# Kernel optimization log

Hardware: AMD Instinct MI355X
Metric: run time of the kernel (lower is better)

## Reference

```python
import jax, jax.numpy as jnp
import numpy as np

D = 768   # embedding_len
NL = 4    # nleft attributes
NR = 4    # nright attributes
LL = 256  # total left tokens
LR = 256  # total right tokens
DE = (NL + NR) * D  # entity-matching highway width


def setup_inputs() -> dict:
    key = jax.random.key(0)
    ks = jax.random.split(key, 12)
    f = lambda k, s: (jax.random.normal(k, s, jnp.float32) * 0.02)
    return {
        "left_emb": jax.random.normal(ks[0], (LL, D), jnp.float32),
        "right_emb": jax.random.normal(ks[1], (LR, D), jnp.float32),
        "Wn_tok": f(ks[2], (D, D)), "bn_tok": jnp.zeros((D,), jnp.float32),
        "Wg_tok": f(ks[3], (D, D)), "bg_tok": jnp.full((D,), -2.0, jnp.float32),
        "W_lin_tok": f(ks[4], (D, 1)), "b_lin_tok": jnp.zeros((1,), jnp.float32),
        "attr_emb_left": f(ks[5], (NL, D)),
        "attr_emb_right": f(ks[6], (NR, D)),
        "Wn_ent": f(ks[7], (DE, DE)), "bn_ent": jnp.zeros((DE,), jnp.float32),
        "Wg_ent": f(ks[8], (DE, DE)), "bg_ent": jnp.full((DE,), -2.0, jnp.float32),
        "W_lin_ent": f(ks[9], (DE, 2)), "b_lin_ent": jnp.zeros((2,), jnp.float32),
        "empty_attr_res": f(ks[10], (D,)),
        # per-attribute token counts; left includes an empty attribute
        "left_attrs_len": jnp.array([100, 80, 76, 0], dtype=jnp.int32),
        "right_attrs_len": jnp.array([64, 64, 64, 64], dtype=jnp.int32),
    }


def _highway(x, Wn, bn, Wg, bg):
    h = jax.nn.relu(x @ Wn + bn)
    g = jax.nn.sigmoid(x @ Wg + bg)
    return h * g + (1.0 - g) * x


def _token_matching(left, right, Wn, bn, Wg, bg, W_lin, b_lin):
    # compare_matrix: [L_left, L_right, D]
    cmp = jnp.abs(left[:, None, :] - right[None, :, :])
    hw = _highway(cmp, Wn, bn, Wg, bg)
    scores = hw @ W_lin + b_lin                     # [Ll, Lr, 1]
    # softmax over dim=1 (right tokens); only argmax is used downstream
    idx = jnp.argmax(scores[..., 0], axis=1)        # [Ll]
    return jnp.take_along_axis(cmp, idx[:, None, None], axis=1)[:, 0, :]  # [Ll, D]


def _attribute_matching(tokens, field_emb, cmp_res, lens, empty_attr):
    # ragged per-attribute softmax-weighted segment reduction
    n = field_emb.shape[0]
    L = tokens.shape[0]
    seg = jnp.repeat(jnp.arange(n), lens, total_repeat_length=L)   # [L]
    scores = jnp.einsum('ld,ld->l', tokens, field_emb[seg])        # [L]
    m = jax.ops.segment_max(scores, seg, num_segments=n)
    e = jnp.exp(scores - m[seg])
    z = jax.ops.segment_sum(e, seg, num_segments=n)
    w = e / z[seg]                                                  # softmax within segment
    reps = jax.ops.segment_sum(w[:, None] * cmp_res, seg, num_segments=n)  # [n, D]
    return jnp.where(lens[:, None] > 0, reps, empty_attr[None, :])


def reference(left_emb, right_emb, Wn_tok, bn_tok, Wg_tok, bg_tok,
              W_lin_tok, b_lin_tok, attr_emb_left, attr_emb_right,
              Wn_ent, bn_ent, Wg_ent, bg_ent, W_lin_ent, b_lin_ent,
              empty_attr_res, left_attrs_len, right_attrs_len):
    left_cmp = _token_matching(left_emb, right_emb, Wn_tok, bn_tok, Wg_tok, bg_tok,
                               W_lin_tok, b_lin_tok)
    right_cmp = _token_matching(right_emb, left_emb, Wn_tok, bn_tok, Wg_tok, bg_tok,
                                W_lin_tok, b_lin_tok)
    left_rep = _attribute_matching(left_emb, attr_emb_left, left_cmp,
                                   left_attrs_len, empty_attr_res)
    right_rep = _attribute_matching(right_emb, attr_emb_right, right_cmp,
                                    right_attrs_len, empty_attr_res)
    concat = jnp.concatenate([left_rep, right_rep], axis=0).reshape(1, -1)  # [1, DE]
    hw = _highway(concat, Wn_ent, bn_ent, Wg_ent, bg_ent)
    logits = hw @ W_lin_ent + b_lin_ent                                     # [1, 2]
    return jax.nn.softmax(logits, axis=1).flatten()                         # [2]
```

## Files before the change

### kernel.cpp

```cpp
#include <hip/hip_runtime.h>
#include <math.h>
#include <stdint.h>

#define DD 768
#define NT 256
#define DE 6144

typedef _Float16 half8 __attribute__((ext_vector_type(8)));
typedef _Float16 half4 __attribute__((ext_vector_type(4)));
typedef short short8 __attribute__((ext_vector_type(8)));
typedef float floatx4 __attribute__((ext_vector_type(4)));

__device__ __forceinline__ void async_ld16(const void* g, void* l) {
  __builtin_amdgcn_global_load_lds(
      (const __attribute__((address_space(1))) unsigned int*)g,
      (__attribute__((address_space(3))) unsigned int*)l, 16, 0, 0);
}

__device__ __forceinline__ unsigned ordf(float f) {
  unsigned u = __float_as_uint(f);
  return (u & 0x80000000u) ? ~u : (u | 0x80000000u);
}

__global__ __launch_bounds__(256) void prep(
    const float* __restrict__ Wn, const float* __restrict__ Wg,
    _Float16* __restrict__ WnT, _Float16* __restrict__ WgT,
    const float* __restrict__ L, const float* __restrict__ R,
    _Float16* __restrict__ Lh, _Float16* __restrict__ Rh)
{
  const int b = blockIdx.x;
  if (b < 1152) {
    const int z = b / 576;
    const int by = (b / 24) % 24;
    const int bx = b % 24;
    const float* W = z ? Wg : Wn;
    _Float16* WT = z ? WgT : WnT;
    __shared__ float tile[32][33];
    const int tx = threadIdx.x & 31, ty = threadIdx.x >> 5;
    const int d0 = bx * 32, k0 = by * 32;
    #pragma unroll
    for (int p = 0; p < 4; ++p)
      tile[ty + p*8][tx] = W[(size_t)(k0 + ty + p*8)*DD + d0 + tx];
    __syncthreads();
    #pragma unroll
    for (int p = 0; p < 4; ++p) {
      const int d = d0 + ty + p*8;
      const int k = k0 + tx;
      const int idx = d*DD + (k & ~63) + ((((k >> 3) & 7) ^ (d & 7)) << 3) + (k & 7);
      WT[idx] = (_Float16)tile[tx][ty + p*8];
    }
  } else {
    const int c = b - 1152;
    const int side = c / 192;
    const float* src = side ? R : L;
    _Float16* dst = side ? Rh : Lh;
    const int o = (c % 192)*1024 + threadIdx.x*4;
    float4 v = *(const float4*)&src[o];
    half4 h; h[0] = (_Float16)v.x; h[1] = (_Float16)v.y;
    h[2] = (_Float16)v.z; h[3] = (_Float16)v.w;
    *(half4*)&dst[o] = h;
  }
}

__global__ __launch_bounds__(512, 1) void score_mfma(
    const _Float16* __restrict__ Lh, const _Float16* __restrict__ Rh,
    const _Float16* __restrict__ WnT, const _Float16* __restrict__ WgT,
    const float* __restrict__ bn, const float* __restrict__ bg,
    const float* __restrict__ Wl, float* __restrict__ Sp)
{
  const int dbase = blockIdx.x * 128;
  const int i     = blockIdx.y;
  const int tid   = threadIdx.x;

  __shared__ _Float16 As [2][256*64];
  __shared__ _Float16 Bns[2][128*64];
  __shared__ _Float16 Bgs[2][128*64];

  floatx4 accn[4][4] = {};
  floatx4 accg[4][4] = {};

  const int kg = tid & 7;
  const int rl = tid >> 3;

  const int lane = tid & 63;
  const int wid  = tid >> 6;
  const int wj = (wid & 3) * 64;
  const int wd = (wid >> 2) * 64;
  const int m = lane & 15;
  const int q = lane >> 4;
  const int gq8 = ((q ^ (m & 7)) << 3);

  const int drow = lane >> 3;
  const int dseg = lane & 7;

  int arow[4], brow[4];
  #pragma unroll
  for (int t4 = 0; t4 < 4; ++t4) {
    arow[t4] = (wj + t4*16 + m) * 64;
    brow[t4] = (wd + t4*16 + m) * 64;
  }

  auto stageB = [&](int k0, int c) {
    #pragma unroll
    for (int tt = 0; tt < 2; ++tt) {
      const int brow0 = wid*16 + tt*8;
      async_ld16(&WnT[(size_t)(dbase + brow0 + drow)*DD + k0 + dseg*8],
                 &Bns[c][brow0*64]);
      async_ld16(&WgT[(size_t)(dbase + brow0 + drow)*DD + k0 + dseg*8],
                 &Bgs[c][brow0*64]);
    }
  };

  stageB(0, 0);
  {
    half8 lh0 = *(const half8*)&Lh[i*DD + kg*8];
    #pragma unroll
    for (int rep = 0; rep < 4; ++rep) {
      const int row = rl + rep*64;
      half8 rv0 = *(const half8*)&Rh[(size_t)row*DD + kg*8];
      half8 dv8 = lh0 - rv0;
      short8 sb; __builtin_memcpy(&sb, &dv8, 16);
      sb &= (short)0x7FFF;
      *(short8*)&As[0][row*64 + ((kg ^ (row & 7)) << 3)] = sb;
    }
  }
  __syncthreads();

  for (int t = 0; t < 12; ++t) {
    const int cur = t & 1;
    const bool st = (t < 11);
    const int k0n = (t + 1) * 64;

    half8 rv[4], lh;
    if (st) {
      stageB(k0n, cur ^ 1);
      __builtin_amdgcn_sched_barrier(0);
      lh = *(const half8*)&Lh[i*DD + k0n + kg*8];
      #pragma unroll
      for (int rep = 0; rep < 4; ++rep)
        rv[rep] = *(const half8*)&Rh[(size_t)(rl + rep*64)*DD + k0n + kg*8];
      __builtin_amdgcn_sched_barrier(0);
    }

    half8 af[4][2];
    #pragma unroll
    for (int tj = 0; tj < 4; ++tj)
      #pragma unroll
      for (int kk = 0; kk < 2; ++kk)
        af[tj][kk] = *(const half8*)&As[cur][arow[tj] + ((kk*32) ^ gq8)];
    __builtin_amdgcn_s_setprio(1);
    #pragma unroll
    for (int td = 0; td < 4; ++td) {
      half8 bn_[2], bg_[2];
      #pragma unroll
      for (int kk = 0; kk < 2; ++kk) {
        bn_[kk] = *(const half8*)&Bns[cur][brow[td] + ((kk*32) ^ gq8)];
        bg_[kk] = *(const half8*)&Bgs[cur][brow[td] + ((kk*32) ^ gq8)];
      }
      #pragma unroll
      for (int kk = 0; kk < 2; ++kk)
        #pragma unroll
        for (int tj = 0; tj < 4; ++tj) {
          accn[tj][td] = __builtin_amdgcn_mfma_f32_16x16x32_f16(
              af[tj][kk], bn_[kk], accn[tj][td], 0, 0, 0);
          accg[tj][td] = __builtin_amdgcn_mfma_f32_16x16x32_f16(
              af[tj][kk], bg_[kk], accg[tj][td], 0, 0, 0);
        }
    }
    __builtin_amdgcn_s_setprio(0);

    if (st) {
      #pragma unroll
      for (int rep = 0; rep < 4; ++rep) {
        const int row = rl + rep*64;
        half8 dv8 = lh - rv[rep];
        short8 sb; __builtin_memcpy(&sb, &dv8, 16);
        sb &= (short)0x7FFF;
        *(short8*)&As[cur ^ 1][row*64 + ((kg ^ (row & 7)) << 3)] = sb;
      }
    }
    __syncthreads();
  }

  float bnv[4], bgv[4], wlv[4], lv[4];
  int dv[4];
  #pragma unroll
  for (int td = 0; td < 4; ++td) {
    const int d = dbase + wd + td*16 + m;
    dv[td] = d; bnv[td] = bn[d]; bgv[td] = bg[d]; wlv[td] = Wl[d];
    lv[td] = (float)Lh[i*DD + d];
  }
  const int jb = wj;
  const int plane = blockIdx.x * 2 + (wid >> 2);
  float* Sout = Sp + (size_t)plane * NT * NT + (size_t)i * NT;
  #pragma unroll
  for (int tj = 0; tj < 4; ++tj) {
    #pragma unroll
    for (int r = 0; r < 4; ++r) {
      const int j = jb + tj*16 + q*4 + r;
      float sc = 0.f;
      #pragma unroll
      for (int td = 0; td < 4; ++td) {
        const float nv = accn[tj][td][r] + bnv[td];
        const float gp = accg[tj][td][r] + bgv[td];
        const float g  = 1.f / (1.f + __expf(-gp));
        const float c  = fabsf(lv[td] - (float)Rh[(size_t)j*DD + dv[td]]);
        sc += (fmaxf(nv, 0.f)*g + (1.f - g)*c) * wlv[td];
      }
      sc += __shfl_xor(sc, 1, 16);
      sc += __shfl_xor(sc, 2, 16);
      sc += __shfl_xor(sc, 4, 16);
      sc += __shfl_xor(sc, 8, 16);
      if (m == 0) Sout[j] = sc;
    }
  }
}

__global__ __launch_bounds__(256) void argmax_attr(
    const float* __restrict__ Sp,
    int* __restrict__ idxL, unsigned long long* __restrict__ colKey,
    const float* __restrict__ Lemb, const float* __restrict__ Remb,
    const float* __restrict__ AEl, const float* __restrict__ AEr,
    const int* __restrict__ lensL, const int* __restrict__ lensR,
    float* __restrict__ wS, int* __restrict__ segA)
{
  const int b = blockIdx.x;
  const int t = threadIdx.x;

  if (b < NT) {
    const size_t off = (size_t)b*NT + t;
    float v = 0.f;
    #pragma unroll
    for (int p = 0; p < 12; ++p) v += Sp[(size_t)p*NT*NT + off];
    const unsigned long long key =
        ((unsigned long long)ordf(v) << 32) | (unsigned)(NT - 1 - b);
    atomicMax(&colKey[t], key);
    int idx = t;
    #pragma unroll
    for (int mm = 1; mm < 64; mm <<= 1) {
      float ov = __shfl_xor(v, mm, 64);
      int   oi = __shfl_xor(idx, mm, 64);
      if (ov > v || (ov == v && oi < idx)) { v = ov; idx = oi; }
    }
    __shared__ float sv[4]; __shared__ int si[4];
    if ((t & 63) == 0) { sv[t>>6] = v; si[t>>6] = idx; }
    __syncthreads();
    if (t == 0) {
      #pragma unroll
      for (int w = 1; w < 4; ++w)
        if (sv[w] > v || (sv[w] == v && si[w] < idx)) { v = sv[w]; idx = si[w]; }
      idxL[b] = idx;
    }
    return;
  }

  const int side = b - NT;
  const float* tok = side ? Remb : Lemb;
  const float* AE  = side ? AEr  : AEl;
  const int* lens  = side ? lensR : lensL;
  const int c0 = lens[0], c1 = c0 + lens[1], c2 = c1 + lens[2];
  const int seg = (t < c0) ? 0 : (t < c1) ? 1 : (t < c2) ? 2 : 3;
  float s = 0.f;
  const float4* tr = (const float4*)&tok[(size_t)t*DD];
  const float4* ar = (const float4*)&AE[(size_t)seg*DD];
  for (int k = 0; k < DD/4; ++k) {
    float4 a = tr[k], bb = ar[k];
    s += a.x*bb.x + a.y*bb.y + a.z*bb.z + a.w*bb.w;
  }
  __shared__ float scS[NT]; __shared__ int segS[NT];
  __shared__ float mS[4], zS[4];
  scS[t] = s; segS[t] = seg;
  __syncthreads();
  if (t < 4) {
    float mx = -INFINITY;
    for (int u = 0; u < NT; ++u) if (segS[u] == t) mx = fmaxf(mx, scS[u]);
    mS[t] = mx;
    float z = 0.f;
    for (int u = 0; u < NT; ++u) if (segS[u] == t) z += __expf(scS[u] - mx);
    zS[t] = z;
  }
  __syncthreads();
  wS[side*NT + t] = __expf(s - mS[seg]) / zS[seg];
  segA[side*NT + t] = seg;
}

__global__ __launch_bounds__(256) void attr_reduce(
    const float* __restrict__ Lemb, const float* __restrict__ Remb,
    const int* __restrict__ lensL, const int* __restrict__ lensR,
    const int* __restrict__ idxL, const unsigned long long* __restrict__ colKey,
    const float* __restrict__ wS, const int* __restrict__ segA,
    const float* __restrict__ empty, float* __restrict__ x)
{
  const int side = blockIdx.x;
  const float* tok = side ? Remb : Lemb;
  const float* oth = side ? Lemb : Remb;
  const int* lens  = side ? lensR : lensL;
  const float* w   = wS + side*NT;
  const int* sg    = segA + side*NT;
  float* xo = x + side*4*DD;
  const int t = threadIdx.x;
  const int dl = t & 63, uq = t >> 6;
  const int d = blockIdx.y*64 + dl;
  float a0 = 0.f, a1 = 0.f, a2 = 0.f, a3 = 0.f;
  for (int u = uq*64; u < uq*64 + 64; ++u) {
    const int iu = side ? (NT - 1 - (int)(unsigned)(colKey[u] & 0xffffffffULL))
                        : idxL[u];
    const float c = fabsf(tok[(size_t)u*DD + d] - oth[(size_t)iu*DD + d]);
    const float wc = w[u] * c;
    const int s = sg[u];
    a0 += (s == 0) ? wc : 0.f;
    a1 += (s == 1) ? wc : 0.f;
    a2 += (s == 2) ? wc : 0.f;
    a3 += (s == 3) ? wc : 0.f;
  }
  __shared__ float red[4][4][64];
  red[uq][0][dl] = a0; red[uq][1][dl] = a1;
  red[uq][2][dl] = a2; red[uq][3][dl] = a3;
  __syncthreads();
  if (uq == 0) {
    #pragma unroll
    for (int s = 0; s < 4; ++s) {
      float v = red[0][s][dl] + red[1][s][dl] + red[2][s][dl] + red[3][s][dl];
      xo[s*DD + d] = (lens[s] > 0) ? v : empty[d];
    }
  }
}

__global__ __launch_bounds__(256) void ent_matvec4(
    const float* __restrict__ x,
    const float* __restrict__ Wn, const float* __restrict__ Wg,
    float* __restrict__ pn, float* __restrict__ pg)
{
  const float* W = blockIdx.z ? Wg : Wn;
  float* p = blockIdx.z ? pg : pn;
  __shared__ float xs[96];
  const int db = blockIdx.x;
  const int kb = blockIdx.y;
  const int tid = threadIdx.x;
  if (tid < 96) xs[tid] = x[kb*96 + tid];
  __syncthreads();
  const int col = db*1024 + tid*4;
  float4 a = {0.f,0.f,0.f,0.f};
  const size_t base = (size_t)kb*96*DE + col;
  #pragma unroll 8
  for (int kk = 0; kk < 96; ++kk) {
    const float xv = xs[kk];
    float4 w = *(const float4*)&W[base + (size_t)kk*DE];
    a.x = fmaf(xv, w.x, a.x); a.y = fmaf(xv, w.y, a.y);
    a.z = fmaf(xv, w.z, a.z); a.w = fmaf(xv, w.w, a.w);
  }
  *(float4*)&p[(size_t)kb*DE + col] = a;
}

__global__ __launch_bounds__(256) void ent_reduce(
    const float* __restrict__ pn, const float* __restrict__ pg,
    float* __restrict__ yn, float* __restrict__ yg)
{
  const int o = blockIdx.x*256 + threadIdx.x;
  float sn = 0.f, sg = 0.f;
  for (int kb = 0; kb < 64; ++kb) {
    sn += pn[(size_t)kb*DE + o];
    sg += pg[(size_t)kb*DE + o];
  }
  yn[o] = sn; yg[o] = sg;
}

__global__ __launch_bounds__(256) void final_kernel(
    const float* __restrict__ x, const float* __restrict__ yn,
    const float* __restrict__ yg, const float* __restrict__ bn,
    const float* __restrict__ bg, const float* __restrict__ Wl,
    const float* __restrict__ bl, float* __restrict__ out)
{
  const int tid = threadIdx.x;
  float a0 = 0.f, a1 = 0.f;
  for (int p = 0; p < DE/256; ++p) {
    int d = p*256 + tid;
    float n  = yn[d] + bn[d];
    float gp = yg[d] + bg[d];
    float h  = fmaxf(n, 0.f);
    float g  = 1.f / (1.f + __expf(-gp));
    float hw = h*g + (1.f - g)*x[d];
    a0 += hw * Wl[d*2 + 0];
    a1 += hw * Wl[d*2 + 1];
  }
  #pragma unroll
  for (int mm = 1; mm < 64; mm <<= 1) {
    a0 += __shfl_xor(a0, mm, 64);
    a1 += __shfl_xor(a1, mm, 64);
  }
  __shared__ float s0[4], s1[4];
  if ((tid & 63) == 0) { s0[tid>>6] = a0; s1[tid>>6] = a1; }
  __syncthreads();
  if (tid == 0) {
    for (int w = 1; w < 4; ++w) { a0 += s0[w]; a1 += s1[w]; }
    float l0 = a0 + bl[0], l1 = a1 + bl[1];
    float m = fmaxf(l0, l1);
    float e0 = __expf(l0 - m), e1 = __expf(l1 - m);
    out[0] = e0 / (e0 + e1);
    out[1] = e1 / (e0 + e1);
  }
}

extern "C" void kernel_launch(void* const* d_in, const int* in_sizes, int n_in,
                              void* d_out, int out_size, void* d_ws, size_t ws_size,
                              hipStream_t stream) {
  const float* Lemb   = (const float*)d_in[0];
  const float* Remb   = (const float*)d_in[1];
  const float* Wn_tok = (const float*)d_in[2];
  const float* bn_tok = (const float*)d_in[3];
  const float* Wg_tok = (const float*)d_in[4];
  const float* bg_tok = (const float*)d_in[5];
  const float* Wl_tok = (const float*)d_in[6];
  const float* AEl    = (const float*)d_in[8];
  const float* AEr    = (const float*)d_in[9];
  const float* Wn_ent = (const float*)d_in[10];
  const float* bn_ent = (const float*)d_in[11];
  const float* Wg_ent = (const float*)d_in[12];
  const float* bg_ent = (const float*)d_in[13];
  const float* Wl_ent = (const float*)d_in[14];
  const float* bl_ent = (const float*)d_in[15];
  const float* empty  = (const float*)d_in[16];
  const int*   lensL  = (const int*)d_in[17];
  const int*   lensR  = (const int*)d_in[18];

  char* ws = (char*)d_ws;
  float* Sp   = (float*)(ws + 0);
  float* pn   = (float*)(ws + 0);
  float* pg   = (float*)(ws + 1572864);
  unsigned long long* colKey = (unsigned long long*)(ws + 3145728);
  float* x    = (float*)(ws + 3147776);
  float* yn   = (float*)(ws + 3172352);
  float* yg   = (float*)(ws + 3196928);
  float* wSm  = (float*)(ws + 3221504);
  int*  segA  = (int*)  (ws + 3223552);
  _Float16* WnT = (_Float16*)(ws + 3225600);
  _Float16* WgT = (_Float16*)(ws + 4405248);
  _Float16* Lh  = (_Float16*)(ws + 5584896);
  _Float16* Rh  = (_Float16*)(ws + 5978112);
  int* idxL = (int*)(ws + 3225600);

  prep<<<1536, 256, 0, stream>>>(Wn_tok, Wg_tok, WnT, WgT, Lemb, Remb, Lh, Rh);
  hipMemsetAsync(colKey, 0, 2048, stream);
  score_mfma<<<dim3(6, 256), 512, 0, stream>>>(
      Lh, Rh, WnT, WgT, bn_tok, bg_tok, Wl_tok, Sp);
  argmax_attr<<<NT + 2, 256, 0, stream>>>(
      Sp, idxL, colKey, Lemb, Remb, AEl, AEr, lensL, lensR, wSm, segA);
  attr_reduce<<<dim3(2, 12), 256, 0, stream>>>(
      Lemb, Remb, lensL, lensR, idxL, colKey, wSm, segA, empty, x);
  ent_matvec4<<<dim3(6, 64, 2), 256, 0, stream>>>(x, Wn_ent, Wg_ent, pn, pg);
  ent_reduce<<<24, 256, 0, stream>>>(pn, pg, yn, yg);
  final_kernel<<<1, 256, 0, stream>>>(
      x, yn, yg, bn_ent, bg_ent, Wl_ent, bl_ent, (float*)d_out);
}
```

Measured before the change: 664.0 us.

## Fuse tail kernels into one cooperative kernel with grid syncs

Replaces the five tail launches (argmax/attr scores, attr_reduce, entity matvec, reduce, final) with a single cooperative kernel of 512 blocks that separates the stages with grid.sync. It also folds the colKey memset into the prep kernel. The aim is to remove launch gaps and a memset call. In exchange it adds grid-wide barrier overhead, and the work is spread over fewer blocks, e.g. the matvec now runs 768 work items on 512 blocks.

```diff
diff --git a/kernel.cpp b/kernel.cpp
--- a/kernel.cpp
+++ b/kernel.cpp
@@ -1,10 +1,13 @@
 #include <hip/hip_runtime.h>
+#include <hip/hip_cooperative_groups.h>
 #include <math.h>
 #include <stdint.h>
 
 #define DD 768
 #define NT 256
 #define DE 6144
+
+namespace cg = cooperative_groups;
 
 typedef _Float16 half8 __attribute__((ext_vector_type(8)));
 typedef _Float16 half4 __attribute__((ext_vector_type(4)));
@@ -26,7 +29,8 @@
     const float* __restrict__ Wn, const float* __restrict__ Wg,
     _Float16* __restrict__ WnT, _Float16* __restrict__ WgT,
     const float* __restrict__ L, const float* __restrict__ R,
-    _Float16* __restrict__ Lh, _Float16* __restrict__ Rh)
+    _Float16* __restrict__ Lh, _Float16* __restrict__ Rh,
+    unsigned long long* __restrict__ colKey)
 {
   const int b = blockIdx.x;
   if (b < 1152) {
@@ -50,6 +54,7 @@
       WT[idx] = (_Float16)tile[tx][ty + p*8];
     }
   } else {
+    if (b == 1152) colKey[threadIdx.x] = 0ULL;
     const int c = b - 1152;
     const int side = c / 192;
     const float* src = side ? R : L;
@@ -216,16 +221,31 @@
   }
 }
 
-__global__ __launch_bounds__(256) void argmax_attr(
+__global__ __launch_bounds__(256) void tail_coop(
     const float* __restrict__ Sp,
     int* __restrict__ idxL, unsigned long long* __restrict__ colKey,
     const float* __restrict__ Lemb, const float* __restrict__ Remb,
     const float* __restrict__ AEl, const float* __restrict__ AEr,
     const int* __restrict__ lensL, const int* __restrict__ lensR,
-    float* __restrict__ wS, int* __restrict__ segA)
+    float* __restrict__ wS, int* __restrict__ segA,
+    const float* __restrict__ empty, float* __restrict__ x,
+    const float* __restrict__ Wn_ent, const float* __restrict__ Wg_ent,
+    float* __restrict__ pn, float* __restrict__ pg,
+    float* __restrict__ yn, float* __restrict__ yg,
+    const float* __restrict__ bn_ent, const float* __restrict__ bg_ent,
+    const float* __restrict__ Wl_ent, const float* __restrict__ bl_ent,
+    float* __restrict__ out)
 {
+  cg::grid_group grid = cg::this_grid();
   const int b = blockIdx.x;
   const int t = threadIdx.x;
+
+  __shared__ float sv[4]; __shared__ int si[4];
+  __shared__ float scS[NT]; __shared__ int segS[NT];
+  __shared__ float mS[4], zS[4];
+  __shared__ float red[4][4][64];
+  __shared__ float xs[96];
+  __shared__ float s0[4], s1[4];
 
   if (b < NT) {
     const size_t off = (size_t)b*NT + t;
@@ -242,7 +262,6 @@
       int   oi = __shfl_xor(idx, mm, 64);
       if (ov > v || (ov == v && oi < idx)) { v = ov; idx = oi; }
     }
-    __shared__ float sv[4]; __shared__ int si[4];
     if ((t & 63) == 0) { sv[t>>6] = v; si[t>>6] = idx; }
     __syncthreads();
     if (t == 0) {
@@ -251,153 +270,142 @@
         if (sv[w] > v || (sv[w] == v && si[w] < idx)) { v = sv[w]; idx = si[w]; }
       idxL[b] = idx;
     }
-    return;
-  }
-
-  const int side = b - NT;
-  const float* tok = side ? Remb : Lemb;
-  const float* AE  = side ? AEr  : AEl;
-  const int* lens  = side ? lensR : lensL;
-  const int c0 = lens[0], c1 = c0 + lens[1], c2 = c1 + lens[2];
-  const int seg = (t < c0) ? 0 : (t < c1) ? 1 : (t < c2) ? 2 : 3;
-  float s = 0.f;
-  const float4* tr = (const float4*)&tok[(size_t)t*DD];
-  const float4* ar = (const float4*)&AE[(size_t)seg*DD];
-  for (int k = 0; k < DD/4; ++k) {
-    float4 a = tr[k], bb = ar[k];
-    s += a.x*bb.x + a.y*bb.y + a.z*bb.z + a.w*bb.w;
-  }
-  __shared__ float scS[NT]; __shared__ int segS[NT];
-  __shared__ float mS[4], zS[4];
-  scS[t] = s; segS[t] = seg;
-  __syncthreads();
-  if (t < 4) {
-    float mx = -INFINITY;
-    for (int u = 0; u < NT; ++u) if (segS[u] == t) mx = fmaxf(mx, scS[u]);
-    mS[t] = mx;
-    float z = 0.f;
-    for (int u = 0; u < NT; ++u) if (segS[u] == t) z += __expf(scS[u] - mx);
-    zS[t] = z;
-  }
-  __syncthreads();
-  wS[side*NT + t] = __expf(s - mS[seg]) / zS[seg];
-  segA[side*NT + t] = seg;
-}
-
-__global__ __launch_bounds__(256) void attr_reduce(
-    const float* __restrict__ Lemb, const float* __restrict__ Remb,
-    const int* __restrict__ lensL, const int* __restrict__ lensR,
-    const int* __restrict__ idxL, const unsigned long long* __restrict__ colKey,
-    const float* __restrict__ wS, const int* __restrict__ segA,
-    const float* __restrict__ empty, float* __restrict__ x)
-{
-  const int side = blockIdx.x;
-  const float* tok = side ? Remb : Lemb;
-  const float* oth = side ? Lemb : Remb;
-  const int* lens  = side ? lensR : lensL;
-  const float* w   = wS + side*NT;
-  const int* sg    = segA + side*NT;
-  float* xo = x + side*4*DD;
-  const int t = threadIdx.x;
-  const int dl = t & 63, uq = t >> 6;
-  const int d = blockIdx.y*64 + dl;
-  float a0 = 0.f, a1 = 0.f, a2 = 0.f, a3 = 0.f;
-  for (int u = uq*64; u < uq*64 + 64; ++u) {
-    const int iu = side ? (NT - 1 - (int)(unsigned)(colKey[u] & 0xffffffffULL))
-                        : idxL[u];
-    const float c = fabsf(tok[(size_t)u*DD + d] - oth[(size_t)iu*DD + d]);
-    const float wc = w[u] * c;
-    const int s = sg[u];
-    a0 += (s == 0) ? wc : 0.f;
-    a1 += (s == 1) ? wc : 0.f;
-    a2 += (s == 2) ? wc : 0.f;
-    a3 += (s == 3) ? wc : 0.f;
-  }
-  __shared__ float red[4][4][64];
-  red[uq][0][dl] = a0; red[uq][1][dl] = a1;
-  red[uq][2][dl] = a2; red[uq][3][dl] = a3;
-  __syncthreads();
-  if (uq == 0) {
-    #pragma unroll
-    for (int s = 0; s < 4; ++s) {
-      float v = red[0][s][dl] + red[1][s][dl] + red[2][s][dl] + red[3][s][dl];
-      xo[s*DD + d] = (lens[s] > 0) ? v : empty[d];
-    }
-  }
-}
-
-__global__ __launch_bounds__(256) void ent_matvec4(
-    const float* __restrict__ x,
-    const float* __restrict__ Wn, const float* __restrict__ Wg,
-    float* __restrict__ pn, float* __restrict__ pg)
-{
-  const float* W = blockIdx.z ? Wg : Wn;
-  float* p = blockIdx.z ? pg : pn;
-  __shared__ float xs[96];
-  const int db = blockIdx.x;
-  const int kb = blockIdx.y;
-  const int tid = threadIdx.x;
-  if (tid < 96) xs[tid] = x[kb*96 + tid];
-  __syncthreads();
-  const int col = db*1024 + tid*4;
-  float4 a = {0.f,0.f,0.f,0.f};
-  const size_t base = (size_t)kb*96*DE + col;
-  #pragma unroll 8
-  for (int kk = 0; kk < 96; ++kk) {
-    const float xv = xs[kk];
-    float4 w = *(const float4*)&W[base + (size_t)kk*DE];
-    a.x = fmaf(xv, w.x, a.x); a.y = fmaf(xv, w.y, a.y);
-    a.z = fmaf(xv, w.z, a.z); a.w = fmaf(xv, w.w, a.w);
-  }
-  *(float4*)&p[(size_t)kb*DE + col] = a;
-}
-
-__global__ __launch_bounds__(256) void ent_reduce(
-    const float* __restrict__ pn, const float* __restrict__ pg,
-    float* __restrict__ yn, float* __restrict__ yg)
-{
-  const int o = blockIdx.x*256 + threadIdx.x;
-  float sn = 0.f, sg = 0.f;
-  for (int kb = 0; kb < 64; ++kb) {
-    sn += pn[(size_t)kb*DE + o];
-    sg += pg[(size_t)kb*DE + o];
-  }
-  yn[o] = sn; yg[o] = sg;
-}
-
-__global__ __launch_bounds__(256) void final_kernel(
-    const float* __restrict__ x, const float* __restrict__ yn,
-    const float* __restrict__ yg, const float* __restrict__ bn,
-    const float* __restrict__ bg, const float* __restrict__ Wl,
-    const float* __restrict__ bl, float* __restrict__ out)
-{
-  const int tid = threadIdx.x;
-  float a0 = 0.f, a1 = 0.f;
-  for (int p = 0; p < DE/256; ++p) {
-    int d = p*256 + tid;
-    float n  = yn[d] + bn[d];
-    float gp = yg[d] + bg[d];
-    float h  = fmaxf(n, 0.f);
-    float g  = 1.f / (1.f + __expf(-gp));
-    float hw = h*g + (1.f - g)*x[d];
-    a0 += hw * Wl[d*2 + 0];
-    a1 += hw * Wl[d*2 + 1];
-  }
+  } else if (b < NT + 2) {
+    const int side = b - NT;
+    const float* tok = side ? Remb : Lemb;
+    const float* AE  = side ? AEr  : AEl;
+    const int* lens  = side ? lensR : lensL;
+    const int c0 = lens[0], c1 = c0 + lens[1], c2 = c1 + lens[2];
+    const int seg = (t < c0) ? 0 : (t < c1) ? 1 : (t < c2) ? 2 : 3;
+    float s = 0.f;
+    const float4* tr = (const float4*)&tok[(size_t)t*DD];
+    const float4* ar = (const float4*)&AE[(size_t)seg*DD];
+    for (int k = 0; k < DD/4; ++k) {
+      float4 a = tr[k], bb = ar[k];
+      s += a.x*bb.x + a.y*bb.y + a.z*bb.z + a.w*bb.w;
+    }
+    scS[t] = s; segS[t] = seg;
+    __syncthreads();
+    if (t < 4) {
+      float mx = -INFINITY;
+      for (int u = 0; u < NT; ++u) if (segS[u] == t) mx = fmaxf(mx, scS[u]);
+      mS[t] = mx;
+      float z = 0.f;
+      for (int u = 0; u < NT; ++u) if (segS[u] == t) z += __expf(scS[u] - mx);
+      zS[t] = z;
+    }
+    __syncthreads();
+    wS[side*NT + t] = __expf(s - mS[seg]) / zS[seg];
+    segA[side*NT + t] = seg;
+  }
+  __threadfence();
+  grid.sync();
+
+  if (b < 24) {
+    const int side = b & 1;
+    const int dblk = b >> 1;
+    const float* tok = side ? Remb : Lemb;
+    const float* oth = side ? Lemb : Remb;
+    const int* lens  = side ? lensR : lensL;
+    const float* w   = wS + side*NT;
+    const int* sg    = segA + side*NT;
+    float* xo = x + side*4*DD;
+    const int dl = t & 63, uq = t >> 6;
+    const int d = dblk*64 + dl;
+    float a0 = 0.f, a1 = 0.f, a2 = 0.f, a3 = 0.f;
+    for (int u = uq*64; u < uq*64 + 64; ++u) {
+      const int iu = side ? (NT - 1 - (int)(unsigned)(colKey[u] & 0xffffffffULL))
+                          : idxL[u];
+      const float c = fabsf(tok[(size_t)u*DD + d] - oth[(size_t)iu*DD + d]);
+      const float wc = w[u] * c;
+      const int s = sg[u];
+      a0 += (s == 0) ? wc : 0.f;
+      a1 += (s == 1) ? wc : 0.f;
+      a2 += (s == 2) ? wc : 0.f;
+      a3 += (s == 3) ? wc : 0.f;
+    }
+    red[uq][0][dl] = a0; red[uq][1][dl] = a1;
+    red[uq][2][dl] = a2; red[uq][3][dl] = a3;
+    __syncthreads();
+    if (uq == 0) {
+      #pragma unroll
+      for (int s = 0; s < 4; ++s) {
+        float v = red[0][s][dl] + red[1][s][dl] + red[2][s][dl] + red[3][s][dl];
+        xo[s*DD + d] = (lens[s] > 0) ? v : empty[d];
+      }
+    }
+  }
+  __threadfence();
+  grid.sync();
+
   #pragma unroll
-  for (int mm = 1; mm < 64; mm <<= 1) {
-    a0 += __shfl_xor(a0, mm, 64);
-    a1 += __shfl_xor(a1, mm, 64);
-  }
-  __shared__ float s0[4], s1[4];
-  if ((tid & 63) == 0) { s0[tid>>6] = a0; s1[tid>>6] = a1; }
-  __syncthreads();
-  if (tid == 0) {
-    for (int w = 1; w < 4; ++w) { a0 += s0[w]; a1 += s1[w]; }
-    float l0 = a0 + bl[0], l1 = a1 + bl[1];
-    float m = fmaxf(l0, l1);
-    float e0 = __expf(l0 - m), e1 = __expf(l1 - m);
-    out[0] = e0 / (e0 + e1);
-    out[1] = e1 / (e0 + e1);
+  for (int rep = 0; rep < 2; ++rep) {
+    const int u = b + rep*512;
+    if (u < 768) {
+      const int mat = u / 384;
+      const int rem = u % 384;
+      const int kb  = rem / 6;
+      const int db  = rem % 6;
+      const float* W = mat ? Wg_ent : Wn_ent;
+      float* p = mat ? pg : pn;
+      __syncthreads();
+      if (t < 96) xs[t] = x[kb*96 + t];
+      __syncthreads();
+      const int col = db*1024 + t*4;
+      float4 a = {0.f,0.f,0.f,0.f};
+      const size_t base = (size_t)kb*96*DE + col;
+      #pragma unroll 8
+      for (int kk = 0; kk < 96; ++kk) {
+        const float xv = xs[kk];
+        float4 w = *(const float4*)&W[base + (size_t)kk*DE];
+        a.x = fmaf(xv, w.x, a.x); a.y = fmaf(xv, w.y, a.y);
+        a.z = fmaf(xv, w.z, a.z); a.w = fmaf(xv, w.w, a.w);
+      }
+      *(float4*)&p[(size_t)kb*DE + col] = a;
+    }
+  }
+  __threadfence();
+  grid.sync();
+
+  if (b < 24) {
+    const int o = b*256 + t;
+    float sn = 0.f, sg = 0.f;
+    for (int kb = 0; kb < 64; ++kb) {
+      sn += pn[(size_t)kb*DE + o];
+      sg += pg[(size_t)kb*DE + o];
+    }
+    yn[o] = sn; yg[o] = sg;
+  }
+  __threadfence();
+  grid.sync();
+
+  if (b == 0) {
+    float a0 = 0.f, a1 = 0.f;
+    for (int p = 0; p < DE/256; ++p) {
+      int d = p*256 + t;
+      float n  = yn[d] + bn_ent[d];
+      float gp = yg[d] + bg_ent[d];
+      float h  = fmaxf(n, 0.f);
+      float g  = 1.f / (1.f + __expf(-gp));
+      float hw = h*g + (1.f - g)*x[d];
+      a0 += hw * Wl_ent[d*2 + 0];
+      a1 += hw * Wl_ent[d*2 + 1];
+    }
+    #pragma unroll
+    for (int mm = 1; mm < 64; mm <<= 1) {
+      a0 += __shfl_xor(a0, mm, 64);
+      a1 += __shfl_xor(a1, mm, 64);
+    }
+    if ((t & 63) == 0) { s0[t>>6] = a0; s1[t>>6] = a1; }
+    __syncthreads();
+    if (t == 0) {
+      for (int w = 1; w < 4; ++w) { a0 += s0[w]; a1 += s1[w]; }
+      float l0 = a0 + bl_ent[0], l1 = a1 + bl_ent[1];
+      float m = fmaxf(l0, l1);
+      float e0 = __expf(l0 - m), e1 = __expf(l1 - m);
+      out[0] = e0 / (e0 + e1);
+      out[1] = e1 / (e0 + e1);
+    }
   }
 }
 
@@ -438,17 +446,22 @@
   _Float16* Lh  = (_Float16*)(ws + 5584896);
   _Float16* Rh  = (_Float16*)(ws + 5978112);
   int* idxL = (int*)(ws + 3225600);
-
-  prep<<<1536, 256, 0, stream>>>(Wn_tok, Wg_tok, WnT, WgT, Lemb, Remb, Lh, Rh);
-  hipMemsetAsync(colKey, 0, 2048, stream);
+  float* outp = (float*)d_out;
+
+  prep<<<1536, 256, 0, stream>>>(Wn_tok, Wg_tok, WnT, WgT, Lemb, Remb, Lh, Rh,
+                                 colKey);
   score_mfma<<<dim3(6, 256), 512, 0, stream>>>(
       Lh, Rh, WnT, WgT, bn_tok, bg_tok, Wl_tok, Sp);
-  argmax_attr<<<NT + 2, 256, 0, stream>>>(
-      Sp, idxL, colKey, Lemb, Remb, AEl, AEr, lensL, lensR, wSm, segA);
-  attr_reduce<<<dim3(2, 12), 256, 0, stream>>>(
-      Lemb, Remb, lensL, lensR, idxL, colKey, wSm, segA, empty, x);
-  ent_matvec4<<<dim3(6, 64, 2), 256, 0, stream>>>(x, Wn_ent, Wg_ent, pn, pg);
-  ent_reduce<<<24, 256, 0, stream>>>(pn, pg, yn, yg);
-  final_kernel<<<1, 256, 0, stream>>>(
-      x, yn, yg, bn_ent, bg_ent, Wl_ent, bl_ent, (float*)d_out);
-}
+
+  void* args[] = {
+    (void*)&Sp, (void*)&idxL, (void*)&colKey,
+    (void*)&Lemb, (void*)&Remb, (void*)&AEl, (void*)&AEr,
+    (void*)&lensL, (void*)&lensR, (void*)&wSm, (void*)&segA,
+    (void*)&empty, (void*)&x, (void*)&Wn_ent, (void*)&Wg_ent,
+    (void*)&pn, (void*)&pg, (void*)&yn, (void*)&yg,
+    (void*)&bn_ent, (void*)&bg_ent, (void*)&Wl_ent, (void*)&bl_ent,
+    (void*)&outp
+  };
+  hipLaunchCooperativeKernel((const void*)tail_coop, dim3(512), dim3(256),
+                             args, 0, stream);
+}
```

Measured after the change: 1.095 ms. +64.9%, slower.
